# Performance work log

Measured on AMD Instinct MI355X. Metric: run time of the kernel, lower is better.

## Reference

```python
import jax, jax.numpy as jnp
import numpy as np

N, D = 8192, 128
TEMPERATURE = 0.07
EPS = 1e-8
NEG_FILL = -9e15


def setup_inputs() -> dict:
    key = jax.random.key(0)
    feats = jax.random.normal(key, (N, D), dtype=jnp.float32)
    # SimCLR-style positive-pair mask: row i's positive is row (i + N//2) % N.
    # Exactly one positive per row, as required by the original broadcast.
    label = jnp.roll(jnp.eye(N, dtype=jnp.int32), N // 2, axis=1)
    return {"feats": feats, "label": label}


def reference(feats, label):
    # F.cosine_similarity clamps each norm at eps before dividing.
    norms = jnp.linalg.norm(feats, axis=-1, keepdims=True)
    nf = feats / jnp.maximum(norms, EPS)            # [N, D] unit rows
    cos_sim = nf @ nf.T                             # [N, N] cosine similarities
    n = cos_sim.shape[0]
    self_mask = jnp.eye(n, dtype=bool)
    cos_sim = jnp.where(self_mask, NEG_FILL, cos_sim)
    cos_sim = cos_sim / TEMPERATURE
    pos_mask = (label == 1)
    # Exactly one positive per row -> masked sum == cos_sim[pos_mask] in row order.
    pos = jnp.sum(jnp.where(pos_mask, cos_sim, 0.0), axis=-1)  # [N]
    lse = jax.nn.logsumexp(cos_sim, axis=-1)                    # [N]
    return jnp.mean(-pos + lse)
```

## Files before the change

kernel.cpp:

```cpp
#include <hip/hip_runtime.h>


#define NN 8192
#define DD 128

typedef __bf16 bf16x8 __attribute__((ext_vector_type(8)));
typedef float f32x4 __attribute__((ext_vector_type(4)));
typedef unsigned int u32x4 __attribute__((ext_vector_type(4)));

constexpr float kM     = 1.0f / 0.07f;
constexpr float kScale = 1.4426950408889634f / 0.07f;
constexpr float kLn2   = 0.6931471805599453f;

__device__ inline unsigned short f2bf(float f) {
  unsigned int u = __float_as_uint(f);
  unsigned int r = (u + 0x7FFFu + ((u >> 16) & 1u)) >> 16;
  return (unsigned short)r;
}

__global__ __launch_bounds__(256) void k_normalize(const float* __restrict__ feats,
                                                   unsigned short* __restrict__ nfb) {
  int tid = threadIdx.x;
  int lane = tid & 63;
  int row = blockIdx.x * 4 + (tid >> 6);
  float2 f = *(const float2*)(feats + (size_t)row * DD + lane * 2);
  float ss = f.x * f.x + f.y * f.y;
  #pragma unroll
  for (int m = 1; m < 64; m <<= 1) ss += __shfl_xor(ss, m);
  float rn = 1.0f / fmaxf(sqrtf(ss), 1e-8f);
  unsigned int lo = f2bf(f.x * rn), hi = f2bf(f.y * rn);
  *(unsigned int*)(nfb + (size_t)row * DD + lane * 2) = lo | (hi << 16);
}

__global__ __launch_bounds__(256) void k_fused(const unsigned short* __restrict__ nfb,
                                               const int* __restrict__ label,
                                               float* __restrict__ lpart,
                                               int* __restrict__ pos_idx) {
  __shared__ __align__(16) unsigned short ldsB[64 * DD];
  int b = blockIdx.x;
  int tid = threadIdx.x;
  int sub = ((b >> 4) << 3) | (b & 7);
  if (b & 8) {
    int g = sub;
    int r0 = (g >> 2) * 64;
    int c0 = (g & 3) * 2048;
    int lane = tid & 63, w = tid >> 6;
    int wm = w >> 1, wn = w & 1;
    int lg = lane >> 4;
    int ll = lane & 15;

    bf16x8 afr[2][4];
    #pragma unroll
    for (int ms = 0; ms < 2; ms++) {
      const unsigned short* arow = nfb + (size_t)(r0 + wm * 32 + ms * 16 + ll) * DD + lg * 8;
      #pragma unroll
      for (int kc = 0; kc < 4; kc++)
        afr[ms][kc] = *(const bf16x8*)(arow + kc * 32);
    }

    float lacc[2][4] = {{0.f, 0.f, 0.f, 0.f}, {0.f, 0.f, 0.f, 0.f}};
    int slr = tid >> 4;
    int sch = tid & 15;

    for (int ct = 0; ct < 32; ct++) {
      int ctile = c0 + ct * 64;
      __syncthreads();
      #pragma unroll
      for (int p = 0; p < 4; p++) {
        int row = p * 16 + slr;
        u32x4 v = *(const u32x4*)(nfb + (size_t)(ctile + row) * DD + sch * 8);
        *(u32x4*)((char*)ldsB + row * 256 + ((sch * 16) ^ ((row & 7) << 4))) = v;
      }
      __syncthreads();

      f32x4 acc[2][2] = {{{0.f,0.f,0.f,0.f},{0.f,0.f,0.f,0.f}},
                         {{0.f,0.f,0.f,0.f},{0.f,0.f,0.f,0.f}}};
      #pragma unroll
      for (int ns = 0; ns < 2; ns++) {
        int brow = wn * 32 + ns * 16 + ll;
        const char* bbase = (const char*)ldsB + brow * 256;
        int sw = (brow & 7) << 4;
        #pragma unroll
        for (int kc = 0; kc < 4; kc++) {
          bf16x8 bfr = *(const bf16x8*)(bbase + ((kc * 64 + lg * 16) ^ sw));
          acc[0][ns] = __builtin_amdgcn_mfma_f32_16x16x32_bf16(afr[0][kc], bfr, acc[0][ns], 0, 0, 0);
          acc[1][ns] = __builtin_amdgcn_mfma_f32_16x16x32_bf16(afr[1][kc], bfr, acc[1][ns], 0, 0, 0);
        }
      }

      bool mayDiag = (ctile < r0 + 64) && (r0 < ctile + 64);
      if (mayDiag) {
        #pragma unroll
        for (int ms = 0; ms < 2; ms++) {
          int growb = r0 + wm * 32 + ms * 16 + lg * 4;
          #pragma unroll
          for (int ns = 0; ns < 2; ns++) {
            int gcol = ctile + wn * 32 + ns * 16 + ll;
            #pragma unroll
            for (int r = 0; r < 4; r++) {
              float s = (growb + r == gcol) ? -3.0e38f : acc[ms][ns][r];
              lacc[ms][r] += __builtin_amdgcn_exp2f((s - 1.0f) * kScale);
            }
          }
        }
      } else {
        #pragma unroll
        for (int ms = 0; ms < 2; ms++)
          #pragma unroll
          for (int ns = 0; ns < 2; ns++)
            #pragma unroll
            for (int r = 0; r < 4; r++)
              lacc[ms][r] += __builtin_amdgcn_exp2f((acc[ms][ns][r] - 1.0f) * kScale);
      }
    }

    #pragma unroll
    for (int ms = 0; ms < 2; ms++)
      #pragma unroll
      for (int r = 0; r < 4; r++) {
        float v = lacc[ms][r];
        v += __shfl_xor(v, 1); v += __shfl_xor(v, 2);
        v += __shfl_xor(v, 4); v += __shfl_xor(v, 8);
        lacc[ms][r] = v;
      }
    if (ll == 0) {
      int slot = (g & 3) * 2 + wn;
      #pragma unroll
      for (int ms = 0; ms < 2; ms++)
        #pragma unroll
        for (int r = 0; r < 4; r++) {
          int grow = r0 + wm * 32 + ms * 16 + lg * 4 + r;
          lpart[(size_t)slot * NN + grow] = lacc[ms][r];
        }
    }
  } else {
    int sg = sub;
    const u32x4* L = (const u32x4*)label;
    int t = sg * 256 + tid;
    for (int k = 0; k < 16; k++) {
      u32x4 v[8];
      #pragma unroll
      for (int j = 0; j < 8; j++)
        v[j] = __builtin_nontemporal_load(&L[t + (k * 8 + j) * 131072]);
      unsigned any = 0;
      #pragma unroll
      for (int j = 0; j < 8; j++) any |= v[j][0] | v[j][1] | v[j][2] | v[j][3];
      if (any) {
        #pragma unroll
        for (int j = 0; j < 8; j++) {
          int idx = t + (k * 8 + j) * 131072;
          if (v[j][0] | v[j][1] | v[j][2] | v[j][3]) {
            int gi = idx * 4;
            int row = gi >> 13, col = gi & (NN - 1);
            if (v[j][0] == 1u) pos_idx[row] = col;
            if (v[j][1] == 1u) pos_idx[row] = col + 1;
            if (v[j][2] == 1u) pos_idx[row] = col + 2;
            if (v[j][3] == 1u) pos_idx[row] = col + 3;
          }
        }
      }
    }
  }
}

__global__ __launch_bounds__(256) void k_finalize(const unsigned short* __restrict__ nfb,
                                                  const float* __restrict__ lpart,
                                                  const int* __restrict__ pos_idx,
                                                  float* __restrict__ bpart) {
  int i = blockIdx.x * 256 + threadIdx.x;
  float l = 0.f;
  #pragma unroll
  for (int s = 0; s < 8; s++) l += lpart[(size_t)s * NN + i];
  float lse = kM + __builtin_amdgcn_logf(l) * kLn2;
  int p = pos_idx[i] & (NN - 1);
  const u32x4* ri = (const u32x4*)(nfb + (size_t)i * DD);
  const u32x4* rp = (const u32x4*)(nfb + (size_t)p * DD);
  float dot = 0.f;
  #pragma unroll
  for (int c = 0; c < 16; c++) {
    u32x4 a = ri[c], bb = rp[c];
    #pragma unroll
    for (int e = 0; e < 4; e++) {
      float al = __uint_as_float(a[e] << 16), ah = __uint_as_float(a[e] & 0xFFFF0000u);
      float bl = __uint_as_float(bb[e] << 16), bh = __uint_as_float(bb[e] & 0xFFFF0000u);
      dot += al * bl + ah * bh;
    }
  }
  float val = lse - dot * kM;
  #pragma unroll
  for (int m = 1; m < 64; m <<= 1) val += __shfl_xor(val, m);
  __shared__ float wsum[4];
  if ((threadIdx.x & 63) == 0) wsum[threadIdx.x >> 6] = val;
  __syncthreads();
  if (threadIdx.x == 0) bpart[blockIdx.x] = wsum[0] + wsum[1] + wsum[2] + wsum[3];
}

__global__ void k_reduce(const float* __restrict__ bpart, float* __restrict__ out) {
  int t = threadIdx.x;
  float v = (t < 32) ? bpart[t] : 0.f;
  #pragma unroll
  for (int m = 1; m < 64; m <<= 1) v += __shfl_xor(v, m);
  if (t == 0) out[0] = v * (1.0f / (float)NN);
}

extern "C" void kernel_launch(void* const* d_in, const int* in_sizes, int n_in,
                              void* d_out, int out_size, void* d_ws, size_t ws_size,
                              hipStream_t stream) {
  (void)in_sizes; (void)n_in; (void)out_size; (void)ws_size;
  const float* feats = (const float*)d_in[0];
  const int* label = (const int*)d_in[1];
  float* out = (float*)d_out;

  char* ws = (char*)d_ws;
  unsigned short* nfb = (unsigned short*)ws;
  float* lpart = (float*)(ws + 2 * 1024 * 1024);
  int* pos_idx = (int*)(ws + 2 * 1024 * 1024 + 262144);
  float* bpart = (float*)(ws + 2 * 1024 * 1024 + 262144 + 32768);

  k_normalize<<<NN / 4, 256, 0, stream>>>(feats, nfb);
  k_fused<<<1024, 256, 0, stream>>>(nfb, label, lpart, pos_idx);
  k_finalize<<<NN / 256, 256, 0, stream>>>(nfb, lpart, pos_idx, bpart);
  k_reduce<<<1, 64, 0, stream>>>(bpart, out);
}
```

Before: 71.28 us.

## Enlarge GEMM row tile to 128, drop reduce kernel via atomic add

The fused block now computes a 128-row by 1024-column slab, with each wave holding four A fragments instead of two. This doubles reuse of every B tile loaded into LDS and halves the number of LDS tile loads per block. Partial LSE slots grow from 8 to 16. The final reduce kernel is replaced by an atomicAdd in finalize plus a memset, launch bounds are dropped, and the label scan uses ordinary loads instead of nontemporal ones. Risks include higher register pressure and lower occupancy from the larger fragment arrays, and a float atomic sum whose order is nondeterministic.

```diff
diff --git a/kernel.cpp b/kernel.cpp
--- a/kernel.cpp
+++ b/kernel.cpp
@@ -32,37 +32,42 @@
   *(unsigned int*)(nfb + (size_t)row * DD + lane * 2) = lo | (hi << 16);
 }
 
-__global__ __launch_bounds__(256) void k_fused(const unsigned short* __restrict__ nfb,
-                                               const int* __restrict__ label,
-                                               float* __restrict__ lpart,
-                                               int* __restrict__ pos_idx) {
+__global__ void k_fused(const unsigned short* __restrict__ nfb,
+                        const int* __restrict__ label,
+                        float* __restrict__ lpart,
+                        int* __restrict__ pos_idx) {
   __shared__ __align__(16) unsigned short ldsB[64 * DD];
   int b = blockIdx.x;
   int tid = threadIdx.x;
   int sub = ((b >> 4) << 3) | (b & 7);
   if (b & 8) {
     int g = sub;
-    int r0 = (g >> 2) * 64;
-    int c0 = (g & 3) * 2048;
+    int r0 = (g >> 3) * 128;
+    int c0 = (g & 7) * 1024;
     int lane = tid & 63, w = tid >> 6;
     int wm = w >> 1, wn = w & 1;
     int lg = lane >> 4;
     int ll = lane & 15;
 
-    bf16x8 afr[2][4];
-    #pragma unroll
-    for (int ms = 0; ms < 2; ms++) {
-      const unsigned short* arow = nfb + (size_t)(r0 + wm * 32 + ms * 16 + ll) * DD + lg * 8;
+    bf16x8 afr[4][4];
+    #pragma unroll
+    for (int ms = 0; ms < 4; ms++) {
+      const unsigned short* arow = nfb + (size_t)(r0 + wm * 64 + ms * 16 + ll) * DD + lg * 8;
       #pragma unroll
       for (int kc = 0; kc < 4; kc++)
         afr[ms][kc] = *(const bf16x8*)(arow + kc * 32);
     }
 
-    float lacc[2][4] = {{0.f, 0.f, 0.f, 0.f}, {0.f, 0.f, 0.f, 0.f}};
+    float lacc[4][4];
+    #pragma unroll
+    for (int ms = 0; ms < 4; ms++)
+      #pragma unroll
+      for (int r = 0; r < 4; r++) lacc[ms][r] = 0.f;
+
     int slr = tid >> 4;
     int sch = tid & 15;
 
-    for (int ct = 0; ct < 32; ct++) {
+    for (int ct = 0; ct < 16; ct++) {
       int ctile = c0 + ct * 64;
       __syncthreads();
       #pragma unroll
@@ -73,8 +78,11 @@
       }
       __syncthreads();
 
-      f32x4 acc[2][2] = {{{0.f,0.f,0.f,0.f},{0.f,0.f,0.f,0.f}},
-                         {{0.f,0.f,0.f,0.f},{0.f,0.f,0.f,0.f}}};
+      f32x4 acc[4][2];
+      #pragma unroll
+      for (int ms = 0; ms < 4; ms++)
+        #pragma unroll
+        for (int ns = 0; ns < 2; ns++) acc[ms][ns] = (f32x4){0.f, 0.f, 0.f, 0.f};
       #pragma unroll
       for (int ns = 0; ns < 2; ns++) {
         int brow = wn * 32 + ns * 16 + ll;
@@ -83,29 +91,30 @@
         #pragma unroll
         for (int kc = 0; kc < 4; kc++) {
           bf16x8 bfr = *(const bf16x8*)(bbase + ((kc * 64 + lg * 16) ^ sw));
-          acc[0][ns] = __builtin_amdgcn_mfma_f32_16x16x32_bf16(afr[0][kc], bfr, acc[0][ns], 0, 0, 0);
-          acc[1][ns] = __builtin_amdgcn_mfma_f32_16x16x32_bf16(afr[1][kc], bfr, acc[1][ns], 0, 0, 0);
-        }
-      }
-
-      bool mayDiag = (ctile < r0 + 64) && (r0 < ctile + 64);
+          #pragma unroll
+          for (int ms = 0; ms < 4; ms++)
+            acc[ms][ns] = __builtin_amdgcn_mfma_f32_16x16x32_bf16(afr[ms][kc], bfr, acc[ms][ns], 0, 0, 0);
+        }
+      }
+
+      bool mayDiag = (ctile < r0 + 128) && (r0 < ctile + 64);
       if (mayDiag) {
         #pragma unroll
-        for (int ms = 0; ms < 2; ms++) {
-          int growb = r0 + wm * 32 + ms * 16 + lg * 4;
+        for (int ms = 0; ms < 4; ms++) {
+          int growb = r0 + wm * 64 + ms * 16 + lg * 4;
           #pragma unroll
           for (int ns = 0; ns < 2; ns++) {
             int gcol = ctile + wn * 32 + ns * 16 + ll;
             #pragma unroll
             for (int r = 0; r < 4; r++) {
-              float s = (growb + r == gcol) ? -3.0e38f : acc[ms][ns][r];
-              lacc[ms][r] += __builtin_amdgcn_exp2f((s - 1.0f) * kScale);
+              float sv = (growb + r == gcol) ? -3.0e38f : acc[ms][ns][r];
+              lacc[ms][r] += __builtin_amdgcn_exp2f((sv - 1.0f) * kScale);
             }
           }
         }
       } else {
         #pragma unroll
-        for (int ms = 0; ms < 2; ms++)
+        for (int ms = 0; ms < 4; ms++)
           #pragma unroll
           for (int ns = 0; ns < 2; ns++)
             #pragma unroll
@@ -115,7 +124,7 @@
     }
 
     #pragma unroll
-    for (int ms = 0; ms < 2; ms++)
+    for (int ms = 0; ms < 4; ms++)
       #pragma unroll
       for (int r = 0; r < 4; r++) {
         float v = lacc[ms][r];
@@ -124,12 +133,12 @@
         lacc[ms][r] = v;
       }
     if (ll == 0) {
-      int slot = (g & 3) * 2 + wn;
-      #pragma unroll
-      for (int ms = 0; ms < 2; ms++)
+      int slot = (g & 7) * 2 + wn;
+      #pragma unroll
+      for (int ms = 0; ms < 4; ms++)
         #pragma unroll
         for (int r = 0; r < 4; r++) {
-          int grow = r0 + wm * 32 + ms * 16 + lg * 4 + r;
+          int grow = r0 + wm * 64 + ms * 16 + lg * 4 + r;
           lpart[(size_t)slot * NN + grow] = lacc[ms][r];
         }
     }
@@ -141,7 +150,7 @@
       u32x4 v[8];
       #pragma unroll
       for (int j = 0; j < 8; j++)
-        v[j] = __builtin_nontemporal_load(&L[t + (k * 8 + j) * 131072]);
+        v[j] = L[t + (k * 8 + j) * 131072];
       unsigned any = 0;
       #pragma unroll
       for (int j = 0; j < 8; j++) any |= v[j][0] | v[j][1] | v[j][2] | v[j][3];
@@ -166,11 +175,11 @@
 __global__ __launch_bounds__(256) void k_finalize(const unsigned short* __restrict__ nfb,
                                                   const float* __restrict__ lpart,
                                                   const int* __restrict__ pos_idx,
-                                                  float* __restrict__ bpart) {
+                                                  float* __restrict__ out) {
   int i = blockIdx.x * 256 + threadIdx.x;
   float l = 0.f;
   #pragma unroll
-  for (int s = 0; s < 8; s++) l += lpart[(size_t)s * NN + i];
+  for (int s = 0; s < 16; s++) l += lpart[(size_t)s * NN + i];
   float lse = kM + __builtin_amdgcn_logf(l) * kLn2;
   int p = pos_idx[i] & (NN - 1);
   const u32x4* ri = (const u32x4*)(nfb + (size_t)i * DD);
@@ -192,15 +201,8 @@
   __shared__ float wsum[4];
   if ((threadIdx.x & 63) == 0) wsum[threadIdx.x >> 6] = val;
   __syncthreads();
-  if (threadIdx.x == 0) bpart[blockIdx.x] = wsum[0] + wsum[1] + wsum[2] + wsum[3];
-}
-
-__global__ void k_reduce(const float* __restrict__ bpart, float* __restrict__ out) {
-  int t = threadIdx.x;
-  float v = (t < 32) ? bpart[t] : 0.f;
-  #pragma unroll
-  for (int m = 1; m < 64; m <<= 1) v += __shfl_xor(v, m);
-  if (t == 0) out[0] = v * (1.0f / (float)NN);
+  if (threadIdx.x == 0)
+    atomicAdd(out, (wsum[0] + wsum[1] + wsum[2] + wsum[3]) * (1.0f / (float)NN));
 }
 
 extern "C" void kernel_launch(void* const* d_in, const int* in_sizes, int n_in,
@@ -214,11 +216,10 @@
   char* ws = (char*)d_ws;
   unsigned short* nfb = (unsigned short*)ws;
   float* lpart = (float*)(ws + 2 * 1024 * 1024);
-  int* pos_idx = (int*)(ws + 2 * 1024 * 1024 + 262144);
-  float* bpart = (float*)(ws + 2 * 1024 * 1024 + 262144 + 32768);
-
+  int* pos_idx = (int*)(ws + 2 * 1024 * 1024 + 524288);
+
+  hipMemsetAsync(out, 0, sizeof(float), stream);
   k_normalize<<<NN / 4, 256, 0, stream>>>(feats, nfb);
   k_fused<<<1024, 256, 0, stream>>>(nfb, label, lpart, pos_idx);
-  k_finalize<<<NN / 256, 256, 0, stream>>>(nfb, lpart, pos_idx, bpart);
-  k_reduce<<<1, 64, 0, stream>>>(bpart, out);
-}
+  k_finalize<<<NN / 256, 256, 0, stream>>>(nfb, lpart, pos_idx, out);
+}
```

Result: slower. 115.1 us (+61.5%).
